# Optimization experiments

Measured on AMD Instinct MI355X. Metric: run time of the kernel, lower is better.

Reference implementation:

```python
import jax, jax.numpy as jnp
import numpy as np

K = 4      # number of per-slot Linear layers (self.k)
H = 512    # hidden_dim
B = 4      # branching factor at every tree level (B >= K -> no padded slots)
T = 1024   # number of trees (roots)
D = 3      # pooled tree levels (= idx_matrix.shape[1] - 2)
N0 = T * B ** D  # 65536 leaves


def _make_level(n_in):
    """Replicates the torch order_matrix / pooling construction for groups of size B.
    order[m, i] = group_base + (pos_in_group + m) % B, then +1 for the zero pad row.
    seg[i] = group id (torch.repeat_interleave of counts)."""
    i = np.arange(n_in)
    base = (i // B) * B
    pos = i % B
    m = np.arange(K)[:, None]
    order = base[None, :] + (pos[None, :] + m) % B + 1  # [K, n_in], all valid since B >= K
    seg = i // B
    return order.astype(np.int32), seg.astype(np.int32)


def setup_inputs() -> dict:
    key = jax.random.key(0)
    ks = jax.random.split(key, 5)
    x = jax.random.normal(ks[0], (N0, H), jnp.float32)
    node_idx = jnp.arange(N0, dtype=jnp.int32)  # idx_matrix[:, -1]
    o1, s1 = _make_level(N0)
    o2, s2 = _make_level(N0 // B)
    o3, s3 = _make_level(N0 // B // B)
    Wz = jax.random.normal(ks[1], (K, H, H), jnp.float32) / np.sqrt(H)   # k slot Linears
    bz = jax.random.normal(ks[2], (K, H), jnp.float32) * 0.02
    Wzf = jax.random.normal(ks[3], (H, H), jnp.float32) / np.sqrt(H)     # z_final_layer
    bzf = jax.random.normal(ks[4], (H,), jnp.float32) * 0.02
    return dict(x=x, Wz=Wz, bz=bz, Wzf=Wzf, bzf=bzf, node_idx=node_idx,
                order1=jnp.asarray(o1), order2=jnp.asarray(o2), order3=jnp.asarray(o3),
                seg1=jnp.asarray(s1), seg2=jnp.asarray(s2), seg3=jnp.asarray(s3))


def _tree_layer(data, order, seg, num_seg, Wz, bz, Wzf, bzf):
    # prepend zero row so padded entries (order == 0) gather zeros
    padded = jnp.concatenate([jnp.zeros((1, data.shape[-1]), data.dtype), data], axis=0)
    emb = padded[order]                                    # [K, N, H] gather
    emb = jnp.einsum('knh,kjh->nkj', emb, Wz) + bz[None]   # per-slot Linear (x @ W.T + b)
    emb = jnp.where((order.T == 0)[..., None], jnp.zeros((), emb.dtype), emb)  # mask padded slots
    emb = emb.sum(axis=1)                                  # sum over K slots -> [N, H]
    emb = emb @ Wzf.T + bzf                                # z_final_layer
    return jax.ops.segment_sum(emb, seg, num_segments=num_seg)  # global_add_pool


def reference(x, Wz, bz, Wzf, bzf, node_idx, order1, order2, order3, seg1, seg2, seg3):
    data = x[node_idx]
    for order, seg in ((order1, seg1), (order2, seg2), (order3, seg3)):
        data = _tree_layer(data, order, seg, order.shape[1] // B, Wz, bz, Wzf, bzf)
    return data  # [T, H]
```

## Files before the change

### kernel.cpp

```cpp
#include <hip/hip_runtime.h>


#define HD 512
#define LDA_T 34
#define LDB_T 68

struct GemmSmem {
    float As[2][32][LDA_T];
    float Bs[2][32][LDB_T];
};

template<int MODE>
__device__ __forceinline__
void gemm_tile(const float* __restrict__ A, const float* __restrict__ B,
               float* __restrict__ C, const float* __restrict__ bias,
               float bscale, int i0, int j0, GemmSmem& sm) {
    const int tid  = threadIdx.x;
    const int tx   = tid & 15, ty = tid >> 4;
    const int arow = tid >> 3, acol4 = (tid & 7) << 2;
    const int ntcol = tid & 63, ntkq = (tid >> 6) << 3;
    const int nncol4 = (tid & 15) << 2, nnk = tid >> 4;

    float4 apre, bpre0, bpre1;

    auto load_tiles = [&](int k0) {
        apre = *(const float4*)&A[(size_t)(i0 + arow) * HD + k0 + acol4];
        if (MODE == 2) {
            const float* bp = &B[(size_t)(j0 + ntcol) * HD + k0 + ntkq];
            bpre0 = *(const float4*)bp;
            bpre1 = *(const float4*)(bp + 4);
        } else if (MODE == 0) {
            bpre0 = *(const float4*)&B[(size_t)(k0 + nnk) * HD + j0 + nncol4];
            bpre1 = *(const float4*)&B[(size_t)(k0 + nnk + 16) * HD + j0 + nncol4];
        } else {
            const float* b0 = &B[(size_t)(k0 + nnk) * HD + j0 + nncol4];
            const float* b1 = &B[(size_t)(k0 + nnk + 16) * HD + j0 + nncol4];
            float4 s0 = *(const float4*)b0, s1 = *(const float4*)b1;
            #pragma unroll
            for (int q = 1; q < 4; ++q) {
                float4 t0 = *(const float4*)(b0 + q * 262144);
                float4 t1 = *(const float4*)(b1 + q * 262144);
                s0.x += t0.x; s0.y += t0.y; s0.z += t0.z; s0.w += t0.w;
                s1.x += t1.x; s1.y += t1.y; s1.z += t1.z; s1.w += t1.w;
            }
            bpre0 = s0; bpre1 = s1;
        }
    };
    auto store_tiles = [&](int buf) {
        sm.As[buf][acol4 + 0][arow] = apre.x;
        sm.As[buf][acol4 + 1][arow] = apre.y;
        sm.As[buf][acol4 + 2][arow] = apre.z;
        sm.As[buf][acol4 + 3][arow] = apre.w;
        if (MODE == 2) {
            sm.Bs[buf][ntkq + 0][ntcol] = bpre0.x;
            sm.Bs[buf][ntkq + 1][ntcol] = bpre0.y;
            sm.Bs[buf][ntkq + 2][ntcol] = bpre0.z;
            sm.Bs[buf][ntkq + 3][ntcol] = bpre0.w;
            sm.Bs[buf][ntkq + 4][ntcol] = bpre1.x;
            sm.Bs[buf][ntkq + 5][ntcol] = bpre1.y;
            sm.Bs[buf][ntkq + 6][ntcol] = bpre1.z;
            sm.Bs[buf][ntkq + 7][ntcol] = bpre1.w;
        } else {
            *(float4*)&sm.Bs[buf][nnk][nncol4]      = bpre0;
            *(float4*)&sm.Bs[buf][nnk + 16][nncol4] = bpre1;
        }
    };

    float acc[2][4] = {};

    load_tiles(0);
    store_tiles(0);
    __syncthreads();

    for (int t = 0; t < 16; ++t) {
        if (t < 15) load_tiles((t + 1) << 5);
        const int cur = t & 1;
        #pragma unroll
        for (int kk = 0; kk < 32; ++kk) {
            float2 av = *(const float2*)&sm.As[cur][kk][ty << 1];
            float4 bv = *(const float4*)&sm.Bs[cur][kk][tx << 2];
            acc[0][0] += av.x * bv.x; acc[0][1] += av.x * bv.y;
            acc[0][2] += av.x * bv.z; acc[0][3] += av.x * bv.w;
            acc[1][0] += av.y * bv.x; acc[1][1] += av.y * bv.y;
            acc[1][2] += av.y * bv.z; acc[1][3] += av.y * bv.w;
        }
        if (t < 15) {
            store_tiles(1 - cur);
            __syncthreads();
        }
    }

    float4 bv = make_float4(0.f, 0.f, 0.f, 0.f);
    if (bias) {
        float4 tb = *(const float4*)&bias[j0 + (tx << 2)];
        bv.x = bscale * tb.x; bv.y = bscale * tb.y;
        bv.z = bscale * tb.z; bv.w = bscale * tb.w;
    }
    #pragma unroll
    for (int r = 0; r < 2; ++r) {
        const int row = i0 + (ty << 1) + r;
        float4 o;
        o.x = acc[r][0] + bv.x; o.y = acc[r][1] + bv.y;
        o.z = acc[r][2] + bv.z; o.w = acc[r][3] + bv.w;
        *(float4*)&C[(size_t)row * HD + j0 + (tx << 2)] = o;
    }
}

__global__ __launch_bounds__(256) void k_stage1(
        const float* __restrict__ x, const float* __restrict__ Wz,
        const float* __restrict__ Wzf, const float* __restrict__ bz,
        const float* __restrict__ bzf,
        float* __restrict__ P3, float* __restrict__ M, float* __restrict__ c0) {
    __shared__ GemmSmem sm;
    const int b = blockIdx.x, tid = threadIdx.x;
    if (b < 512) {
        const int gid  = (b << 8) + tid;
        const int tree = gid >> 7, col4 = gid & 127;
        const float4* xp = (const float4*)x + (size_t)tree * 8192 + col4;
        float4 a0 = make_float4(0,0,0,0), a1 = a0, a2 = a0, a3 = a0;
        #pragma unroll 4
        for (int r = 0; r < 64; r += 4) {
            float4 v0 = xp[(size_t)(r + 0) * 128];
            float4 v1 = xp[(size_t)(r + 1) * 128];
            float4 v2 = xp[(size_t)(r + 2) * 128];
            float4 v3 = xp[(size_t)(r + 3) * 128];
            a0.x += v0.x; a0.y += v0.y; a0.z += v0.z; a0.w += v0.w;
            a1.x += v1.x; a1.y += v1.y; a1.z += v1.z; a1.w += v1.w;
            a2.x += v2.x; a2.y += v2.y; a2.z += v2.z; a2.w += v2.w;
            a3.x += v3.x; a3.y += v3.y; a3.z += v3.z; a3.w += v3.w;
        }
        float4 o;
        o.x = (a0.x + a1.x) + (a2.x + a3.x);
        o.y = (a0.y + a1.y) + (a2.y + a3.y);
        o.z = (a0.z + a1.z) + (a2.z + a3.z);
        o.w = (a0.w + a1.w) + (a2.w + a3.w);
        ((float4*)P3)[gid] = o;
    } else if (b < 640) {
        const int bb = b - 512;
        gemm_tile<1>(Wzf, Wz, M, nullptr, 0.f, (bb >> 3) << 5, (bb & 7) << 6, sm);
    } else {
        float* bs = (float*)&sm;
        if (tid < 128) {
            const int h = tid << 2;
            #pragma unroll
            for (int i = 0; i < 4; ++i)
                bs[h + i] = bz[h + i] + bz[512 + h + i] + bz[1024 + h + i] + bz[1536 + h + i];
        }
        __syncthreads();
        #pragma unroll
        for (int r = 0; r < 2; ++r) {
            const int j = tid + (r << 8);
            float s = 0.f;
            for (int h = 0; h < HD; h += 4) {
                float4 w = *(const float4*)&Wzf[(size_t)j * HD + h];
                s += w.x * bs[h] + w.y * bs[h + 1] + w.z * bs[h + 2] + w.w * bs[h + 3];
            }
            c0[j] = 4.f * (s + bzf[j]);
        }
    }
}

__global__ __launch_bounds__(256) void k_stage2(
        const float* __restrict__ M, const float* __restrict__ P3,
        const float* __restrict__ c0,
        float* __restrict__ M2, float* __restrict__ Y1, float* __restrict__ u) {
    __shared__ GemmSmem sm;
    const int b = blockIdx.x;
    if (b < 128) {
        gemm_tile<0>(M, M, M2, nullptr, 0.f, (b >> 3) << 5, (b & 7) << 6, sm);
    } else if (b < 384) {
        const int bb = b - 128;
        gemm_tile<2>(P3, M, Y1, c0, 16.f, (bb >> 3) << 5, (bb & 7) << 6, sm);
    } else {
        const int j = ((b - 384) << 8) + threadIdx.x;
        float s = 0.f;
        for (int h = 0; h < HD; h += 4) {
            float4 m = *(const float4*)&M[(size_t)j * HD + h];
            float4 c = *(const float4*)&c0[h];
            s += m.x * c.x + m.y * c.y + m.z * c.z + m.w * c.w;
        }
        u[j] = 4.f * s + c0[j];
    }
}

__global__ __launch_bounds__(256) void k_stage3(
        const float* __restrict__ Y1, const float* __restrict__ M2,
        const float* __restrict__ u, float* __restrict__ out) {
    __shared__ GemmSmem sm;
    const int b = blockIdx.x;
    gemm_tile<2>(Y1, M2, out, u, 1.f, (b >> 3) << 5, (b & 7) << 6, sm);
}

extern "C" void kernel_launch(void* const* d_in, const int* in_sizes, int n_in,
                              void* d_out, int out_size, void* d_ws, size_t ws_size,
                              hipStream_t stream) {
    const float* x   = (const float*)d_in[0];
    const float* Wz  = (const float*)d_in[1];
    const float* bz  = (const float*)d_in[2];
    const float* Wzf = (const float*)d_in[3];
    const float* bzf = (const float*)d_in[4];
    float* out = (float*)d_out;

    float* ws = (float*)d_ws;
    float* P3 = ws;
    float* Y1 = ws + 524288;
    float* M  = ws + 1048576;
    float* M2 = ws + 1310720;
    float* c0 = ws + 1572864;
    float* u  = ws + 1573376;

    hipLaunchKernelGGL(k_stage1, dim3(641), dim3(256), 0, stream,
                       x, Wz, Wzf, bz, bzf, P3, M, c0);
    hipLaunchKernelGGL(k_stage2, dim3(386), dim3(256), 0, stream,
                       M, P3, c0, M2, Y1, u);
    hipLaunchKernelGGL(k_stage3, dim3(256), dim3(256), 0, stream,
                       Y1, M2, u, out);
}
```

Baseline: 309.1 us.

## Split pooling into its own kernel and wave-parallelize matvec bias reductions

Moves the leaf-sum pooling out of the fused stage-1 kernel into a dedicated kernel with one block per tree, deeper load batching and a two-half shared-memory reduction. The c0 and u matrix-vector products now give each wave one output row and reduce it with shuffles, which spreads those serial per-thread loops over many blocks. This adds one kernel launch and drops the overlap of pooling with the weight GEMM in exchange for more parallelism in the small tail work.

```diff
diff --git a/kernel.cpp b/kernel.cpp
--- a/kernel.cpp
+++ b/kernel.cpp
@@ -67,7 +67,6 @@
     };
 
     float acc[2][4] = {};
-
     load_tiles(0);
     store_tiles(0);
     __syncthreads();
@@ -106,56 +105,65 @@
     }
 }
 
-__global__ __launch_bounds__(256) void k_stage1(
-        const float* __restrict__ x, const float* __restrict__ Wz,
-        const float* __restrict__ Wzf, const float* __restrict__ bz,
-        const float* __restrict__ bzf,
-        float* __restrict__ P3, float* __restrict__ M, float* __restrict__ c0) {
+__global__ __launch_bounds__(256) void pool_kernel(const float* __restrict__ x,
+                                                   float* __restrict__ P3) {
+    __shared__ float4 red[128];
+    const int tree = blockIdx.x, tid = threadIdx.x;
+    const float4* xp = (const float4*)x + (size_t)tree * 8192 + tid;
+    float4 a0 = make_float4(0.f, 0.f, 0.f, 0.f), a1 = a0;
+    #pragma unroll
+    for (int g = 0; g < 4; ++g) {
+        float4 v[8];
+        #pragma unroll
+        for (int i = 0; i < 8; ++i) v[i] = xp[(size_t)(g * 8 + i) * 256];
+        #pragma unroll
+        for (int i = 0; i < 8; i += 2) {
+            a0.x += v[i].x;     a0.y += v[i].y;
+            a0.z += v[i].z;     a0.w += v[i].w;
+            a1.x += v[i + 1].x; a1.y += v[i + 1].y;
+            a1.z += v[i + 1].z; a1.w += v[i + 1].w;
+        }
+    }
+    a0.x += a1.x; a0.y += a1.y; a0.z += a1.z; a0.w += a1.w;
+    if (tid >= 128) red[tid - 128] = a0;
+    __syncthreads();
+    if (tid < 128) {
+        float4 b = red[tid];
+        a0.x += b.x; a0.y += b.y; a0.z += b.z; a0.w += b.w;
+        ((float4*)P3)[tree * 128 + tid] = a0;
+    }
+}
+
+__global__ __launch_bounds__(256) void pre_kernel(
+        const float* __restrict__ Wz, const float* __restrict__ Wzf,
+        const float* __restrict__ bz, const float* __restrict__ bzf,
+        float* __restrict__ M, float* __restrict__ c0) {
     __shared__ GemmSmem sm;
     const int b = blockIdx.x, tid = threadIdx.x;
-    if (b < 512) {
-        const int gid  = (b << 8) + tid;
-        const int tree = gid >> 7, col4 = gid & 127;
-        const float4* xp = (const float4*)x + (size_t)tree * 8192 + col4;
-        float4 a0 = make_float4(0,0,0,0), a1 = a0, a2 = a0, a3 = a0;
-        #pragma unroll 4
-        for (int r = 0; r < 64; r += 4) {
-            float4 v0 = xp[(size_t)(r + 0) * 128];
-            float4 v1 = xp[(size_t)(r + 1) * 128];
-            float4 v2 = xp[(size_t)(r + 2) * 128];
-            float4 v3 = xp[(size_t)(r + 3) * 128];
-            a0.x += v0.x; a0.y += v0.y; a0.z += v0.z; a0.w += v0.w;
-            a1.x += v1.x; a1.y += v1.y; a1.z += v1.z; a1.w += v1.w;
-            a2.x += v2.x; a2.y += v2.y; a2.z += v2.z; a2.w += v2.w;
-            a3.x += v3.x; a3.y += v3.y; a3.z += v3.z; a3.w += v3.w;
-        }
-        float4 o;
-        o.x = (a0.x + a1.x) + (a2.x + a3.x);
-        o.y = (a0.y + a1.y) + (a2.y + a3.y);
-        o.z = (a0.z + a1.z) + (a2.z + a3.z);
-        o.w = (a0.w + a1.w) + (a2.w + a3.w);
-        ((float4*)P3)[gid] = o;
-    } else if (b < 640) {
-        const int bb = b - 512;
-        gemm_tile<1>(Wzf, Wz, M, nullptr, 0.f, (bb >> 3) << 5, (bb & 7) << 6, sm);
+    if (b < 128) {
+        gemm_tile<1>(Wzf, Wz, M, nullptr, 0.f, (b >> 3) << 5, (b & 7) << 6, sm);
     } else {
-        float* bs = (float*)&sm;
-        if (tid < 128) {
-            const int h = tid << 2;
+        const int bb = b - 128, wave = tid >> 6, lane = tid & 63;
+        const int hb = lane << 3;
+        float4 s0 = *(const float4*)&bz[hb];
+        float4 s1 = *(const float4*)&bz[hb + 4];
+        #pragma unroll
+        for (int q = 1; q < 4; ++q) {
+            float4 t0 = *(const float4*)&bz[q * HD + hb];
+            float4 t1 = *(const float4*)&bz[q * HD + hb + 4];
+            s0.x += t0.x; s0.y += t0.y; s0.z += t0.z; s0.w += t0.w;
+            s1.x += t1.x; s1.y += t1.y; s1.z += t1.z; s1.w += t1.w;
+        }
+        #pragma unroll
+        for (int q = 0; q < 4; ++q) {
+            const int j = bb * 16 + wave * 4 + q;
+            const float4* wr = (const float4*)&Wzf[(size_t)j * HD + hb];
+            float4 w0 = wr[0], w1 = wr[1];
+            float p = w0.x * s0.x + w0.y * s0.y + w0.z * s0.z + w0.w * s0.w
+                    + w1.x * s1.x + w1.y * s1.y + w1.z * s1.z + w1.w * s1.w;
             #pragma unroll
-            for (int i = 0; i < 4; ++i)
-                bs[h + i] = bz[h + i] + bz[512 + h + i] + bz[1024 + h + i] + bz[1536 + h + i];
-        }
-        __syncthreads();
-        #pragma unroll
-        for (int r = 0; r < 2; ++r) {
-            const int j = tid + (r << 8);
-            float s = 0.f;
-            for (int h = 0; h < HD; h += 4) {
-                float4 w = *(const float4*)&Wzf[(size_t)j * HD + h];
-                s += w.x * bs[h] + w.y * bs[h + 1] + w.z * bs[h + 2] + w.w * bs[h + 3];
-            }
-            c0[j] = 4.f * (s + bzf[j]);
+            for (int off = 32; off > 0; off >>= 1) p += __shfl_down(p, off);
+            if (lane == 0) c0[j] = 4.f * (p + bzf[j]);
         }
     }
 }
@@ -165,21 +173,23 @@
         const float* __restrict__ c0,
         float* __restrict__ M2, float* __restrict__ Y1, float* __restrict__ u) {
     __shared__ GemmSmem sm;
-    const int b = blockIdx.x;
+    const int b = blockIdx.x, tid = threadIdx.x;
     if (b < 128) {
         gemm_tile<0>(M, M, M2, nullptr, 0.f, (b >> 3) << 5, (b & 7) << 6, sm);
     } else if (b < 384) {
         const int bb = b - 128;
         gemm_tile<2>(P3, M, Y1, c0, 16.f, (bb >> 3) << 5, (bb & 7) << 6, sm);
     } else {
-        const int j = ((b - 384) << 8) + threadIdx.x;
-        float s = 0.f;
-        for (int h = 0; h < HD; h += 4) {
-            float4 m = *(const float4*)&M[(size_t)j * HD + h];
-            float4 c = *(const float4*)&c0[h];
-            s += m.x * c.x + m.y * c.y + m.z * c.z + m.w * c.w;
-        }
-        u[j] = 4.f * s + c0[j];
+        const int bb = b - 384, wave = tid >> 6, lane = tid & 63;
+        const int j = bb * 4 + wave, hb = lane << 3;
+        const float4* mr = (const float4*)&M[(size_t)j * HD + hb];
+        const float4* cr = (const float4*)&c0[hb];
+        float4 m0 = mr[0], m1 = mr[1], q0 = cr[0], q1 = cr[1];
+        float p = m0.x * q0.x + m0.y * q0.y + m0.z * q0.z + m0.w * q0.w
+                + m1.x * q1.x + m1.y * q1.y + m1.z * q1.z + m1.w * q1.w;
+        #pragma unroll
+        for (int off = 32; off > 0; off >>= 1) p += __shfl_down(p, off);
+        if (lane == 0) u[j] = 4.f * p + c0[j];
     }
 }
 
@@ -209,10 +219,11 @@
     float* c0 = ws + 1572864;
     float* u  = ws + 1573376;
 
-    hipLaunchKernelGGL(k_stage1, dim3(641), dim3(256), 0, stream,
-                       x, Wz, Wzf, bz, bzf, P3, M, c0);
-    hipLaunchKernelGGL(k_stage2, dim3(386), dim3(256), 0, stream,
+    hipLaunchKernelGGL(pool_kernel, dim3(1024), dim3(256), 0, stream, x, P3);
+    hipLaunchKernelGGL(pre_kernel,  dim3(160),  dim3(256), 0, stream,
+                       Wz, Wzf, bz, bzf, M, c0);
+    hipLaunchKernelGGL(k_stage2,    dim3(512),  dim3(256), 0, stream,
                        M, P3, c0, M2, Y1, u);
-    hipLaunchKernelGGL(k_stage3, dim3(256), dim3(256), 0, stream,
+    hipLaunchKernelGGL(k_stage3,    dim3(256),  dim3(256), 0, stream,
                        Y1, M2, u, out);
 }
```

Measured after the change: 314.4 us. No clear change (+1.7%).
